# Optimization experiments

Hardware: AMD Instinct MI355X
Metric: run time of the kernel (lower is better)

The kernel has to match this reference:

```python
import math
import jax, jax.numpy as jnp
import numpy as np

EPS = 1e-4
FMAX = 18  # max filtersize for scale clamped to 2.5: ceil(3*2^2.5+0.5)=18 -> kernel 37x37
KSZ = 2 * FMAX + 1


def _conv2d(x, w, b):
    # 3x3 conv, padding 1, NCHW / OIHW (cross-correlation, matches torch)
    y = jax.lax.conv_general_dilated(x, w, (1, 1), [(1, 1), (1, 1)],
                                     dimension_numbers=('NCHW', 'OIHW', 'NCHW'))
    return y + b[None, :, None, None]


def _basis_filters(scale):
    # scale: [B] -> [B,3,K,K] (g, dgdx, dgdy), masked to the per-sample support
    std = 2.0 ** scale                              # [B]
    fs = jnp.ceil(3.0 * std + 0.5)                  # per-sample filtersize
    x = jnp.arange(-FMAX, FMAX + 1, dtype=jnp.float32)          # [K]
    m = (jnp.abs(x)[None, :] <= fs[:, None]).astype(jnp.float32)  # [B,K] support mask
    e = jnp.exp(-0.5 * (x[None, :] / std[:, None]) ** 2) * m      # masked 1D gaussian [B,K]
    g = e[:, :, None] * e[:, None, :]                              # [B,K,K]
    g = g / jnp.sum(g, axis=(1, 2), keepdims=True)
    c = (-x[None, :] / (std[:, None] ** 3 * 2.0 * math.pi)) * e    # [B,K]
    dgdx = c[:, :, None] * e[:, None, :]   # varies along first spatial dim (x[0])
    dgdx = dgdx / jnp.sum(jnp.abs(dgdx), axis=(1, 2), keepdims=True)
    dgdy = e[:, :, None] * c[:, None, :]   # varies along second spatial dim (x[1])
    dgdy = dgdy / jnp.sum(jnp.abs(dgdy), axis=(1, 2), keepdims=True)
    return jnp.stack([g, dgdx, dgdy], axis=1)  # [B,3,K,K]


def setup_inputs() -> dict:
    key = jax.random.key(0)
    ks = jax.random.split(key, 7)
    B, H, W = 8, 512, 512
    batch = jax.random.uniform(ks[0], (B, 3, H, W), dtype=jnp.float32)
    gcm = jnp.array([[0.06, 0.63, 0.27], [0.3, 0.04, -0.35], [0.34, -0.6, 0.17]],
                    dtype=jnp.float32)
    w1 = jax.random.normal(ks[1], (16, 3, 3, 3), dtype=jnp.float32) * 0.1
    b1 = jax.random.normal(ks[2], (16,), dtype=jnp.float32) * 0.01
    w2 = jax.random.normal(ks[3], (16, 16, 3, 3), dtype=jnp.float32) * 0.1
    b2 = jax.random.normal(ks[4], (16,), dtype=jnp.float32) * 0.01
    w3 = jax.random.normal(ks[5], (1, 16, 3, 3), dtype=jnp.float32) * 0.1
    b3 = jax.random.normal(ks[6], (1,), dtype=jnp.float32) * 0.01
    return {"batch": batch, "gcm": gcm, "w1": w1, "b1": b1,
            "w2": w2, "b2": b2, "w3": w3, "b3": b3}


def reference(batch, gcm, w1, b1, w2, b2, w3, b3):
    B, _, H, W = batch.shape
    # ---- RGB order prior (non-differentiable, no_grad in torch) ----
    oh = lambda i: jax.nn.one_hot(i, 3, axis=1, dtype=batch.dtype)
    mx = jnp.argmax(batch, axis=1)                 # first max
    mn = jnp.argmin(batch, axis=1)
    bf = batch[:, ::-1]
    mx2 = 2 - jnp.argmax(bf, axis=1)               # last max
    mn2 = 2 - jnp.argmin(bf, axis=1)
    RGB_order = jax.lax.stop_gradient(
        0.5 * (oh(mx) + oh(mx2)) - 0.5 * (oh(mn) + oh(mn2)))  # [B,3,H,W]

    # ---- per-sample adaptive scale from small CNN ----
    h = jax.nn.silu(_conv2d(batch, w1, b1))
    h = jax.nn.silu(_conv2d(h, w2, b2))
    s = _conv2d(h, w3, b3)
    scale = jnp.clip(jnp.mean(s, axis=(1, 2, 3)), -2.5, 2.5)   # [B]

    # ---- Gaussian color model ----
    xg = jnp.einsum('ij,bjhw->bihw', gcm, batch)  # [B,3,H,W] -> (E, El, Ell)

    # ---- per-sample Gaussian basis convolution, batched via grouped conv ----
    basis = _basis_filters(scale)                                  # [B,3,K,K]
    xin = xg.reshape(1, B * 3, H, W)
    wk = jnp.broadcast_to(basis[:, None], (B, 3, 3, KSZ, KSZ)).reshape(B * 9, 1, KSZ, KSZ)
    out = jax.lax.conv_general_dilated(xin, wk, (1, 1), [(FMAX, FMAX), (FMAX, FMAX)],
                                       feature_group_count=B * 3,
                                       dimension_numbers=('NCHW', 'OIHW', 'NCHW'))
    out = out.reshape(B, 3, 3, H, W)   # [B, chan(E/El/Ell), filt(g/dx/dy), H, W]
    E = out[:, 0, 0:1]
    Ex = out[:, 0, 1:2]
    Ey = out[:, 0, 2:3]
    El = out[:, 1, 0:1]
    Ell = out[:, 2, 0:1]

    Hf = jnp.arctan(El / (Ell + EPS))
    S = jnp.log((El ** 2 + Ell ** 2) / (E ** 2 + EPS) + EPS)
    Ww = jnp.arctan((Ex / (E + EPS)) ** 2 + (Ey / (E + EPS)) ** 2)
    return jnp.concatenate([Hf, S, RGB_order, Ww], axis=1)  # [B,6,H,W]
```

## Files before the change

kernel.cpp:

```cpp
#include <hip/hip_runtime.h>
#include <hip/hip_bf16.h>

constexpr int BN = 8, HH = 512, WW = 512;
constexpr int PIX = HH * WW;
constexpr float EPSF = 1e-4f;

__device__ __forceinline__ float b2f(__hip_bfloat16 x) { return __bfloat162float(x); }
__device__ __forceinline__ __hip_bfloat16 f2b(float x) { return __float2bfloat16(x); }
__device__ __forceinline__ unsigned short bfbits(float x) {
    union { __hip_bfloat16 b; unsigned short u; } cv; cv.b = f2b(x); return cv.u;
}
__device__ __forceinline__ unsigned int cvtpk(float lo, float hi) {
    unsigned int r;
    asm("v_cvt_pk_bf16_f32 %0, %1, %2" : "=v"(r) : "v"(lo), "v"(hi));
    return r;
}
__device__ __forceinline__ float silu(float a) {
    return a * __builtin_amdgcn_rcpf(1.f + __expf(-a));
}

typedef __attribute__((ext_vector_type(8))) short bf16x8;
typedef __attribute__((ext_vector_type(4))) float f32x4;

constexpr int OFF_TOT = 0;
constexpr int OFF_ROW0 = 128;
constexpr int OFF_ROW1 = 256;
constexpr int OFF_COL0 = 384;
constexpr int OFF_COL1 = 512;
constexpr int OFF_COR = 640;
constexpr int OFF_W1R = 1280;
constexpr int OFF_WR  = 2048;
constexpr int OFF_EH  = 4608;
constexpr int OFF_CH  = 5120;
constexpr size_t OFF_TPB = 65536;
constexpr size_t TP_BYTES = (size_t)4 * BN * PIX * 4;
constexpr size_t WS_NEEDED = OFF_TPB + TP_BYTES;

__global__ void prep_kernel(const float* __restrict__ w1, const float* __restrict__ w2,
                            float* __restrict__ wsf) {
    int t = threadIdx.x;
    for (int i = t; i < 640; i += 256) wsf[i] = 0.f;
    unsigned short* ab = (unsigned short*)(wsf + OFF_WR);
    for (int idx = t; idx < 5120; idx += 256) {
        int part = idx / 2560;
        int id = idx - part * 2560;
        int ks = id >> 9, rem = id & 511, lane = rem >> 3, j = id & 7;
        int oc = lane & 15, q = lane >> 4;
        int k = q * 8 + j;
        int tap = 2 * ks + (k >> 4), ic = k & 15;
        float val = (tap <= 8) ? w2[oc * 144 + ic * 9 + tap] : 0.f;
        float hv = b2f(f2b(val));
        ab[idx] = (part == 0) ? bfbits(val) : bfbits(val - hv);
    }
    unsigned short* a1 = (unsigned short*)(wsf + OFF_W1R);
    for (int idx = t; idx < 1024; idx += 256) {
        int part = idx >> 9;
        int id = idx & 511;
        int lane = id >> 3, j = id & 7;
        int oc = lane & 15, q = lane >> 4;
        int k = q * 8 + j;
        float val = (k < 27) ? w1[oc * 27 + k] : 0.f;
        float hv = b2f(f2b(val));
        a1[idx] = (part == 0) ? bfbits(val) : bfbits(val - hv);
    }
}

__global__ __launch_bounds__(256) void conv12_kernel(const float* __restrict__ batch,
                                                     const unsigned short* __restrict__ w1buf,
                                                     const float* __restrict__ b1,
                                                     const unsigned short* __restrict__ abuf,
                                                     const float* __restrict__ b2v,
                                                     float* __restrict__ wsf,
                                                     float* __restrict__ out) {
    __shared__ float st[3][12][68];
    __shared__ uint4 h1s[10 * 66 * 2];
    __shared__ float part[4][16];

    int tx = threadIdx.x;
    int lane = tx & 63, wave = tx >> 6;
    int n = lane & 15, q = lane >> 4;
    int w0 = blockIdx.x * 64, h0 = blockIdx.y * 8, b = blockIdx.z;

    union { uint4 u; bf16x8 v; } cv;
    const float* pb = batch + (size_t)(b * 3) * PIX;

    for (int i = tx; i < 2448; i += 256) {
        int ch = i / 816;
        int rem = i - ch * 816;
        int r = rem / 68, c = rem - r * 68;
        int gh = h0 - 2 + r, gw = w0 - 2 + c;
        float v = 0.f;
        if (gh >= 0 && gh < HH && gw >= 0 && gw < WW)
            v = pb[(size_t)ch * PIX + (size_t)gh * WW + gw];
        st[ch][r][c] = v;
    }

    bf16x8 w1h, w1l;
    const uint4* w14 = (const uint4*)w1buf;
    cv.u = w14[lane];      w1h = cv.v;
    cv.u = w14[64 + lane]; w1l = cv.v;
    int koff[8];
#pragma unroll
    for (int j = 0; j < 8; j++) {
        int k = q * 8 + j;
        int kk = (k < 27) ? k : 0;
        int ic = kk / 9, rem = kk - ic * 9, kh = rem / 3, kw = rem - kh * 3;
        koff[j] = ic * 816 + kh * 68 + kw;
    }
    float b1q[4];
#pragma unroll
    for (int r = 0; r < 4; r++) b1q[r] = b1[q * 4 + r];
    bool hiq = (q == 3);
    __syncthreads();

    const float* stf = &st[0][0][0];
    unsigned int* hw = (unsigned int*)h1s;
    for (int g = wave; g < 42; g += 4) {
        int i = g * 16 + n; if (i > 659) i = 659;
        int r = i / 66, c = i - r * 66;
        int base = r * 68 + c;
        float x[8];
#pragma unroll
        for (int j = 0; j < 8; j++) x[j] = stf[base + koff[j]];
#pragma unroll
        for (int j = 3; j < 8; j++) x[j] = hiq ? 0.f : x[j];
        union { unsigned int w[4]; bf16x8 v; } bb;
        bb.w[0] = cvtpk(x[0], x[1]);
        bb.w[1] = cvtpk(x[2], x[3]);
        bb.w[2] = cvtpk(x[4], x[5]);
        bb.w[3] = cvtpk(x[6], x[7]);
        f32x4 a = {0, 0, 0, 0};
        a = __builtin_amdgcn_mfma_f32_16x16x32_bf16(w1h, bb.v, a, 0, 0, 0);
        a = __builtin_amdgcn_mfma_f32_16x16x32_bf16(w1l, bb.v, a, 0, 0, 0);
        int gh = h0 - 1 + r, gw = w0 - 1 + c;
        bool ok = ((unsigned)gh < (unsigned)HH) && ((unsigned)gw < (unsigned)WW);
        unsigned int p0 = cvtpk(silu(a[0] + b1q[0]), silu(a[1] + b1q[1]));
        unsigned int p1 = cvtpk(silu(a[2] + b1q[2]), silu(a[3] + b1q[3]));
        p0 = ok ? p0 : 0u;
        p1 = ok ? p1 : 0u;
        int swz = (c >> 2) & 1;
        int slot = i * 2 + ((q >= 2) ? (swz ^ 1) : swz);
        *(uint2*)&hw[slot * 4 + (q & 1) * 2] = make_uint2(p0, p1);
    }

    for (int j = tx; j < 512; j += 256) {
        int rr = j >> 6, ccx = j & 63;
        float v0 = st[0][rr + 2][ccx + 2];
        float v1 = st[1][rr + 2][ccx + 2];
        float v2 = st[2][rr + 2][ccx + 2];
        int mx  = (v0 >= v1 && v0 >= v2) ? 0 : ((v1 >= v2) ? 1 : 2);
        int mx2 = (v2 >= v1 && v2 >= v0) ? 2 : ((v1 >= v0) ? 1 : 0);
        int mn  = (v0 <= v1 && v0 <= v2) ? 0 : ((v1 <= v2) ? 1 : 2);
        int mn2 = (v2 <= v1 && v2 <= v0) ? 2 : ((v1 <= v0) ? 1 : 0);
        size_t p = (size_t)(h0 + rr) * WW + (w0 + ccx);
#pragma unroll
        for (int c = 0; c < 3; c++) {
            float r = 0.5f * ((float)(c == mx) + (float)(c == mx2))
                    - 0.5f * ((float)(c == mn) + (float)(c == mn2));
            out[(size_t)(b * 6 + 2 + c) * PIX + p] = r;
        }
    }
    __syncthreads();

    bf16x8 ah[5], al[5];
    const uint4* ab4 = (const uint4*)abuf;
#pragma unroll
    for (int ks = 0; ks < 5; ks++) {
        cv.u = ab4[ks * 64 + lane];       ah[ks] = cv.v;
        cv.u = ab4[320 + ks * 64 + lane]; al[ks] = cv.v;
    }
    float b2q[4];
#pragma unroll
    for (int r = 0; r < 4; r++) b2q[r] = b2v[q * 4 + r];

    float tt[4] = {0, 0, 0, 0};
    float cs0[4] = {0, 0, 0, 0};
    float cs1[4] = {0, 0, 0, 0};
    for (int rloc = 0; rloc < 2; rloc++) {
        int row = wave * 2 + rloc;
        int grow = h0 + row;
        f32x4 acc[4] = {{0,0,0,0},{0,0,0,0},{0,0,0,0},{0,0,0,0}};
#pragma unroll
        for (int ks = 0; ks < 5; ks++) {
            int tap = 2 * ks + (q >> 1); if (tap > 8) tap = 8;
            int dh = tap / 3 - 1, dw = tap % 3 - 1;
            int half = q & 1;
            int lr = row + 1 + dh;
#pragma unroll
            for (int t = 0; t < 4; t++) {
                int c = 1 + dw + t * 16 + n;
                cv.u = h1s[(lr * 66 + c) * 2 + (half ^ ((c >> 2) & 1))];
                acc[t] = __builtin_amdgcn_mfma_f32_16x16x32_bf16(ah[ks], cv.v, acc[t], 0, 0, 0);
                acc[t] = __builtin_amdgcn_mfma_f32_16x16x32_bf16(al[ks], cv.v, acc[t], 0, 0, 0);
            }
        }
        float sv[4][4];
#pragma unroll
        for (int t = 0; t < 4; t++)
#pragma unroll
            for (int r = 0; r < 4; r++)
                sv[t][r] = silu(acc[t][r] + b2q[r]);
#pragma unroll
        for (int r = 0; r < 4; r++) tt[r] += sv[0][r] + sv[1][r] + sv[2][r] + sv[3][r];
        if (grow == 0 || grow == HH - 1) {
            int off = (grow == 0) ? OFF_ROW0 : OFF_ROW1;
#pragma unroll
            for (int r = 0; r < 4; r++) {
                float x = sv[0][r] + sv[1][r] + sv[2][r] + sv[3][r];
#pragma unroll
                for (int d = 1; d < 16; d <<= 1) x += __shfl_xor(x, d, 64);
                if (n == 0) atomicAdd(&wsf[off + b * 16 + q * 4 + r], x);
            }
        }
        if (blockIdx.x == 0 && n == 0)
#pragma unroll
            for (int r = 0; r < 4; r++) cs0[r] += sv[0][r];
        if (blockIdx.x == 7 && n == 15)
#pragma unroll
            for (int r = 0; r < 4; r++) cs1[r] += sv[3][r];
        if ((grow == 0 || grow == HH - 1)) {
            int hi = (grow == 0) ? 0 : 1;
            if (blockIdx.x == 0 && n == 0)
#pragma unroll
                for (int r = 0; r < 4; r++)
                    wsf[OFF_COR + ((b * 2 + hi) * 2 + 0) * 16 + q * 4 + r] = sv[0][r];
            if (blockIdx.x == 7 && n == 15)
#pragma unroll
                for (int r = 0; r < 4; r++)
                    wsf[OFF_COR + ((b * 2 + hi) * 2 + 1) * 16 + q * 4 + r] = sv[3][r];
        }
    }
    if (blockIdx.x == 0 && n == 0)
#pragma unroll
        for (int r = 0; r < 4; r++) atomicAdd(&wsf[OFF_COL0 + b * 16 + q * 4 + r], cs0[r]);
    if (blockIdx.x == 7 && n == 15)
#pragma unroll
        for (int r = 0; r < 4; r++) atomicAdd(&wsf[OFF_COL1 + b * 16 + q * 4 + r], cs1[r]);
#pragma unroll
    for (int r = 0; r < 4; r++) {
        float x = tt[r];
#pragma unroll
        for (int d = 1; d < 16; d <<= 1) x += __shfl_xor(x, d, 64);
        tt[r] = x;
    }
    if (n == 0)
#pragma unroll
        for (int r = 0; r < 4; r++) part[wave][q * 4 + r] = tt[r];
    __syncthreads();
    if (tx < 16)
        atomicAdd(&wsf[OFF_TOT + b * 16 + tx],
                  part[0][tx] + part[1][tx] + part[2][tx] + part[3][tx]);
}

__global__ void filter_kernel(const float* __restrict__ w3, const float* __restrict__ b3,
                              float* __restrict__ wsf) {
    int b = blockIdx.x, t = threadIdx.x;
    __shared__ float red[160];
    float val = 0.f;
    if (t < 144) {
        int ic = t / 9, tap = t % 9, kh = tap / 3, kw = tap % 3;
        float T = wsf[OFF_TOT + b * 16 + ic];
        int hi = -1, wi = -1;
        if (kh == 0) { T -= wsf[OFF_ROW1 + b * 16 + ic]; hi = 1; }
        else if (kh == 2) { T -= wsf[OFF_ROW0 + b * 16 + ic]; hi = 0; }
        if (kw == 0) { T -= wsf[OFF_COL1 + b * 16 + ic]; wi = 1; }
        else if (kw == 2) { T -= wsf[OFF_COL0 + b * 16 + ic]; wi = 0; }
        if (hi >= 0 && wi >= 0) T += wsf[OFF_COR + ((b * 2 + hi) * 2 + wi) * 16 + ic];
        val = w3[t] * T;
    }
    red[t] = val;
    __syncthreads();
    __shared__ float sh_mean;
    if (t == 0) {
        float S = 0.f;
        for (int i = 0; i < 144; i++) S += red[i];
        sh_mean = b3[0] + S * (1.f / (float)PIX);
    }
    __syncthreads();
    float scale = fminf(2.5f, fmaxf(-2.5f, sh_mean));
    float sd = exp2f(scale);
    float fs = ceilf(3.f * sd + 0.5f);
    float e = 0.f, c = 0.f;
    if (t < 37) {
        float x = (float)(t - 18);
        if (fabsf(x) <= fs) {
            float qq = x / sd;
            e = __expf(-0.5f * qq * qq);
            c = -x / (sd * sd * sd * 6.28318530717958647692f) * e;
        }
    }
    __shared__ float sa[40], sb[40];
    if (t < 37) { sa[t] = e; sb[t] = fabsf(c); }
    __syncthreads();
    __shared__ float Se, Sc;
    if (t == 0) {
        float a = 0.f, d = 0.f;
        for (int i = 0; i < 37; i++) { a += sa[i]; d += sb[i]; }
        Se = a; Sc = d;
    }
    __syncthreads();
    if (t < 37) {
        wsf[OFF_EH + b * 37 + t] = e / Se;
        wsf[OFF_CH + b * 37 + t] = c / Sc;
    }
}

__device__ __forceinline__ int skw(int c) { return c + (c >> 5); }
__global__ __launch_bounds__(256, 4) void horiz_kernel(const float* __restrict__ batch,
                                                       const float* __restrict__ gcm,
                                                       const float* __restrict__ ehat,
                                                       const float* __restrict__ chat,
                                                       float* __restrict__ t) {
    __shared__ float xr[2][3][566];
    int tx = threadIdx.x;
    int h0 = blockIdx.x * 2;
    int b  = blockIdx.y;
    const float* pb = batch + (size_t)(b * 3) * PIX;
    float g0 = gcm[0], g1 = gcm[1], g2 = gcm[2];
    float g3 = gcm[3], g4 = gcm[4], g5 = gcm[5];
    float g6 = gcm[6], g7 = gcm[7], g8 = gcm[8];
    for (int i = tx; i < 2 * 548; i += 256) {
        int r = i / 548, c = i - r * 548;
        int gw = c - 18;
        float v0 = 0.f, v1 = 0.f, v2 = 0.f;
        if (gw >= 0 && gw < WW) {
            size_t p = (size_t)(h0 + r) * WW + gw;
            v0 = pb[p]; v1 = pb[(size_t)PIX + p]; v2 = pb[2 * (size_t)PIX + p];
        }
        int cs = skw(c);
        xr[r][0][cs] = g0 * v0 + g1 * v1 + g2 * v2;
        xr[r][1][cs] = g3 * v0 + g4 * v1 + g5 * v2;
        xr[r][2][cs] = g6 * v0 + g7 * v1 + g8 * v2;
    }
    __syncthreads();
    int r = tx >> 7, colbase = (tx & 127) * 4;
    const float* eh = ehat + b * 37; const float* ch = chat + b * 37;
    float a0[4] = {}, a1[4] = {}, a2[4] = {}, a3[4] = {};
#pragma unroll 4
    for (int kk = 0; kk < 40; kk++) {
        int cs = skw(colbase + kk);
        float x0 = xr[r][0][cs], x1 = xr[r][1][cs], x2 = xr[r][2][cs];
#pragma unroll
        for (int i = 0; i < 4; i++) {
            int k = kk - i;
            if (k >= 0 && k < 37) {
                float ce = eh[k], cc = ch[k];
                a0[i] += ce * x0; a1[i] += ce * x1;
                a2[i] += ce * x2; a3[i] += cc * x0;
            }
        }
    }
    const size_t PL = (size_t)BN * PIX;
    size_t p = (size_t)b * PIX + (size_t)(h0 + r) * WW + colbase;
    *(float4*)&t[0 * PL + p] = make_float4(a0[0], a0[1], a0[2], a0[3]);
    *(float4*)&t[1 * PL + p] = make_float4(a1[0], a1[1], a1[2], a1[3]);
    *(float4*)&t[2 * PL + p] = make_float4(a2[0], a2[1], a2[2], a2[3]);
    *(float4*)&t[3 * PL + p] = make_float4(a3[0], a3[1], a3[2], a3[3]);
}

__global__ __launch_bounds__(256, 4) void vert_kernel(const float* __restrict__ t,
                                                      const float* __restrict__ ehat,
                                                      const float* __restrict__ chat,
                                                      float* __restrict__ out) {
    int tx = threadIdx.x;
    int j = blockIdx.x * 64 + (tx & 63);
    int r0 = (blockIdx.y * 4 + (tx >> 6)) * 4;
    int b = blockIdx.z;
    const float* eh = ehat + b * 37; const float* ch = chat + b * 37;
    const size_t PL = (size_t)BN * PIX;
    const float* t0 = t + (size_t)b * PIX;
    float E[4] = {}, Ex[4] = {}, Ey[4] = {}, El[4] = {}, Ell[4] = {};
#pragma unroll 4
    for (int kk = 0; kk < 40; kk++) {
        int gr = r0 - 18 + kk;
        if (gr >= 0 && gr < HH) {
            size_t idx = (size_t)gr * WW + j;
            float v0 = t0[idx], v1 = t0[PL + idx], v2 = t0[2 * PL + idx], v3 = t0[3 * PL + idx];
#pragma unroll
            for (int i = 0; i < 4; i++) {
                int k = kk - i;
                if (k >= 0 && k < 37) {
                    float ce = eh[k], cc = ch[k];
                    E[i] += ce * v0; Ex[i] += cc * v0; Ey[i] += ce * v3;
                    El[i] += ce * v1; Ell[i] += ce * v2;
                }
            }
        }
    }
#pragma unroll
    for (int i = 0; i < 4; i++) {
        int h = r0 + i;
        float Hf = atanf(El[i] / (Ell[i] + EPSF));
        float S = logf((El[i] * El[i] + Ell[i] * Ell[i]) / (E[i] * E[i] + EPSF) + EPSF);
        float rx = Ex[i] / (E[i] + EPSF), ry = Ey[i] / (E[i] + EPSF);
        float Wv = atanf(rx * rx + ry * ry);
        size_t base = (size_t)(b * 6) * PIX + (size_t)h * WW + j;
        out[base] = Hf;
        out[base + PIX] = S;
        out[base + 5 * (size_t)PIX] = Wv;
    }
}

extern "C" void kernel_launch(void* const* d_in, const int* in_sizes, int n_in,
                              void* d_out, int out_size, void* d_ws, size_t ws_size,
                              hipStream_t stream) {
    const float* batch = (const float*)d_in[0];
    const float* gcm   = (const float*)d_in[1];
    const float* w1    = (const float*)d_in[2];
    const float* b1    = (const float*)d_in[3];
    const float* w2    = (const float*)d_in[4];
    const float* b2    = (const float*)d_in[5];
    const float* w3    = (const float*)d_in[6];
    const float* b3    = (const float*)d_in[7];
    float* out = (float*)d_out;

    if (ws_size < WS_NEEDED) return;

    float* wsf = (float*)d_ws;
    float* tpl = (float*)((char*)d_ws + OFF_TPB);
    float* ehat = wsf + OFF_EH;
    float* chat = wsf + OFF_CH;

    prep_kernel<<<dim3(1), dim3(256), 0, stream>>>(w1, w2, wsf);
    conv12_kernel<<<dim3(8, 64, 8), dim3(256), 0, stream>>>(
        batch, (const unsigned short*)(wsf + OFF_W1R), b1,
        (const unsigned short*)(wsf + OFF_WR), b2, wsf, out);
    filter_kernel<<<dim3(8), dim3(160), 0, stream>>>(w3, b3, wsf);
    horiz_kernel<<<dim3(256, 8), dim3(256), 0, stream>>>(batch, gcm, ehat, chat, tpl);
    vert_kernel<<<dim3(8, 32, 8), dim3(256), 0, stream>>>(tpl, ehat, chat, out);
}
```

Measured before the change: 251.5 us.

## Peel separable conv loops, rotate coefficients in registers, add interior fast paths

The horizontal and vertical Gaussian passes now stage the per-sample filter taps in shared memory. Each pass peels its 40-step tap loop into prologue, steady-state and epilogue parts, passing the taps to the four output rows or columns through rotating registers, which removes the per-iteration bounds and index checks. The vertical pass adds an interior-block path with no row-bounds checks. The conv12 kernel loads input rows one per wave, with unchecked loads for non-edge blocks, and its first-layer loop is reorganised by rows so border masking only runs in edge blocks. In exchange there is more code and register pressure, plus one extra block barrier in the vertical kernel.

```diff
diff --git a/kernel.cpp b/kernel.cpp
--- a/kernel.cpp
+++ b/kernel.cpp
@@ -80,19 +80,29 @@
     int lane = tx & 63, wave = tx >> 6;
     int n = lane & 15, q = lane >> 4;
     int w0 = blockIdx.x * 64, h0 = blockIdx.y * 8, b = blockIdx.z;
+    bool edgeB = (blockIdx.x == 0) || (blockIdx.x == 7) || (blockIdx.y == 0) || (blockIdx.y == 63);
 
     union { uint4 u; bf16x8 v; } cv;
     const float* pb = batch + (size_t)(b * 3) * PIX;
 
-    for (int i = tx; i < 2448; i += 256) {
-        int ch = i / 816;
-        int rem = i - ch * 816;
-        int r = rem / 68, c = rem - r * 68;
-        int gh = h0 - 2 + r, gw = w0 - 2 + c;
-        float v = 0.f;
-        if (gh >= 0 && gh < HH && gw >= 0 && gw < WW)
-            v = pb[(size_t)ch * PIX + (size_t)gh * WW + gw];
-        st[ch][r][c] = v;
+    for (int rr = wave; rr < 36; rr += 4) {
+        int ch = rr / 12, r = rr - ch * 12;
+        int gh = h0 - 2 + r;
+        const float* rp = pb + (size_t)ch * PIX + (size_t)gh * WW + (w0 - 2);
+        if (!edgeB) {
+            st[ch][r][lane] = rp[lane];
+            if (lane < 4) st[ch][r][64 + lane] = rp[64 + lane];
+        } else {
+            bool rok = (gh >= 0) && (gh < HH);
+            int gw = w0 - 2 + lane;
+            float v = (rok && gw >= 0 && gw < WW) ? rp[lane] : 0.f;
+            st[ch][r][lane] = v;
+            if (lane < 4) {
+                int gw2 = gw + 64;
+                float v2 = (rok && gw2 >= 0 && gw2 < WW) ? rp[64 + lane] : 0.f;
+                st[ch][r][64 + lane] = v2;
+            }
+        }
     }
 
     bf16x8 w1h, w1l;
@@ -111,14 +121,16 @@
 #pragma unroll
     for (int r = 0; r < 4; r++) b1q[r] = b1[q * 4 + r];
     bool hiq = (q == 3);
+    int swzl = (n >> 2) & 1;
     __syncthreads();
 
     const float* stf = &st[0][0][0];
     unsigned int* hw = (unsigned int*)h1s;
-    for (int g = wave; g < 42; g += 4) {
-        int i = g * 16 + n; if (i > 659) i = 659;
-        int r = i / 66, c = i - r * 66;
-        int base = r * 68 + c;
+    for (int g = wave; g < 50; g += 4) {
+        int row = g / 5, sub = g - row * 5;
+        int c = sub * 16 + n;
+        int cc_ = (c < 66) ? c : 65;
+        int base = row * 68 + cc_;
         float x[8];
 #pragma unroll
         for (int j = 0; j < 8; j++) x[j] = stf[base + koff[j]];
@@ -132,15 +144,18 @@
         f32x4 a = {0, 0, 0, 0};
         a = __builtin_amdgcn_mfma_f32_16x16x32_bf16(w1h, bb.v, a, 0, 0, 0);
         a = __builtin_amdgcn_mfma_f32_16x16x32_bf16(w1l, bb.v, a, 0, 0, 0);
-        int gh = h0 - 1 + r, gw = w0 - 1 + c;
-        bool ok = ((unsigned)gh < (unsigned)HH) && ((unsigned)gw < (unsigned)WW);
         unsigned int p0 = cvtpk(silu(a[0] + b1q[0]), silu(a[1] + b1q[1]));
         unsigned int p1 = cvtpk(silu(a[2] + b1q[2]), silu(a[3] + b1q[3]));
-        p0 = ok ? p0 : 0u;
-        p1 = ok ? p1 : 0u;
-        int swz = (c >> 2) & 1;
-        int slot = i * 2 + ((q >= 2) ? (swz ^ 1) : swz);
-        *(uint2*)&hw[slot * 4 + (q & 1) * 2] = make_uint2(p0, p1);
+        if (edgeB) {
+            int gh = h0 - 1 + row, gw = w0 - 1 + cc_;
+            bool ok = (gh >= 0) && (gh < HH) && (gw >= 0) && (gw < WW);
+            p0 = ok ? p0 : 0u;
+            p1 = ok ? p1 : 0u;
+        }
+        if (c < 66) {
+            int slot = (row * 66 + c) * 2 + ((q >= 2) ? (swzl ^ 1) : swzl);
+            *(uint2*)&hw[slot * 4 + (q & 1) * 2] = make_uint2(p0, p1);
+        }
     }
 
     for (int j = tx; j < 512; j += 256) {
@@ -312,9 +327,11 @@
                                                        const float* __restrict__ chat,
                                                        float* __restrict__ t) {
     __shared__ float xr[2][3][566];
+    __shared__ float cE[40], cC[40];
     int tx = threadIdx.x;
     int h0 = blockIdx.x * 2;
     int b  = blockIdx.y;
+    if (tx < 37) { cE[tx] = ehat[b * 37 + tx]; cC[tx] = chat[b * 37 + tx]; }
     const float* pb = batch + (size_t)(b * 3) * PIX;
     float g0 = gcm[0], g1 = gcm[1], g2 = gcm[2];
     float g3 = gcm[3], g4 = gcm[4], g5 = gcm[5];
@@ -334,21 +351,56 @@
     }
     __syncthreads();
     int r = tx >> 7, colbase = (tx & 127) * 4;
-    const float* eh = ehat + b * 37; const float* ch = chat + b * 37;
     float a0[4] = {}, a1[4] = {}, a2[4] = {}, a3[4] = {};
-#pragma unroll 4
-    for (int kk = 0; kk < 40; kk++) {
+    float e1, e2, e3, d1, d2, d3;
+    {
+        float ce[3], cc2[3];
+#pragma unroll
+        for (int k = 0; k < 3; k++) { ce[k] = cE[k]; cc2[k] = cC[k]; }
+#pragma unroll
+        for (int kk = 0; kk < 3; kk++) {
+            int cs = skw(colbase + kk);
+            float x0 = xr[r][0][cs], x1 = xr[r][1][cs], x2 = xr[r][2][cs];
+#pragma unroll
+            for (int i = 0; i < 3; i++) {
+                if (i <= kk) {
+                    float ce_ = ce[kk - i], cc_ = cc2[kk - i];
+                    a0[i] += ce_ * x0; a1[i] += ce_ * x1;
+                    a2[i] += ce_ * x2; a3[i] += cc_ * x0;
+                }
+            }
+        }
+        e1 = ce[2]; e2 = ce[1]; e3 = ce[0];
+        d1 = cc2[2]; d2 = cc2[1]; d3 = cc2[0];
+    }
+#pragma unroll 2
+    for (int kk = 3; kk < 37; kk++) {
+        float e0 = cE[kk], d0 = cC[kk];
         int cs = skw(colbase + kk);
         float x0 = xr[r][0][cs], x1 = xr[r][1][cs], x2 = xr[r][2][cs];
-#pragma unroll
-        for (int i = 0; i < 4; i++) {
-            int k = kk - i;
-            if (k >= 0 && k < 37) {
-                float ce = eh[k], cc = ch[k];
-                a0[i] += ce * x0; a1[i] += ce * x1;
-                a2[i] += ce * x2; a3[i] += cc * x0;
-            }
-        }
+        a0[0] += e0 * x0; a1[0] += e0 * x1; a2[0] += e0 * x2; a3[0] += d0 * x0;
+        a0[1] += e1 * x0; a1[1] += e1 * x1; a2[1] += e1 * x2; a3[1] += d1 * x0;
+        a0[2] += e2 * x0; a1[2] += e2 * x1; a2[2] += e2 * x2; a3[2] += d2 * x0;
+        a0[3] += e3 * x0; a1[3] += e3 * x1; a2[3] += e3 * x2; a3[3] += d3 * x0;
+        e3 = e2; e2 = e1; e1 = e0; d3 = d2; d2 = d1; d1 = d0;
+    }
+    {
+        int cs = skw(colbase + 37);
+        float x0 = xr[r][0][cs], x1 = xr[r][1][cs], x2 = xr[r][2][cs];
+        a0[1] += e1 * x0; a1[1] += e1 * x1; a2[1] += e1 * x2; a3[1] += d1 * x0;
+        a0[2] += e2 * x0; a1[2] += e2 * x1; a2[2] += e2 * x2; a3[2] += d2 * x0;
+        a0[3] += e3 * x0; a1[3] += e3 * x1; a2[3] += e3 * x2; a3[3] += d3 * x0;
+    }
+    {
+        int cs = skw(colbase + 38);
+        float x0 = xr[r][0][cs], x1 = xr[r][1][cs], x2 = xr[r][2][cs];
+        a0[2] += e1 * x0; a1[2] += e1 * x1; a2[2] += e1 * x2; a3[2] += d1 * x0;
+        a0[3] += e2 * x0; a1[3] += e2 * x1; a2[3] += e2 * x2; a3[3] += d2 * x0;
+    }
+    {
+        int cs = skw(colbase + 39);
+        float x0 = xr[r][0][cs], x1 = xr[r][1][cs], x2 = xr[r][2][cs];
+        a0[3] += e1 * x0; a1[3] += e1 * x1; a2[3] += e1 * x2; a3[3] += d1 * x0;
     }
     const size_t PL = (size_t)BN * PIX;
     size_t p = (size_t)b * PIX + (size_t)(h0 + r) * WW + colbase;
@@ -358,34 +410,82 @@
     *(float4*)&t[3 * PL + p] = make_float4(a3[0], a3[1], a3[2], a3[3]);
 }
 
+#define VACC(ee, dd, ii) { E[ii] += (ee) * v0; Ex[ii] += (dd) * v0; Ey[ii] += (ee) * v3; \
+                           El[ii] += (ee) * v1; Ell[ii] += (ee) * v2; }
 __global__ __launch_bounds__(256, 4) void vert_kernel(const float* __restrict__ t,
                                                       const float* __restrict__ ehat,
                                                       const float* __restrict__ chat,
                                                       float* __restrict__ out) {
+    __shared__ float cE[40], cC[40];
     int tx = threadIdx.x;
+    int b = blockIdx.z;
+    if (tx < 37) { cE[tx] = ehat[b * 37 + tx]; cC[tx] = chat[b * 37 + tx]; }
     int j = blockIdx.x * 64 + (tx & 63);
     int r0 = (blockIdx.y * 4 + (tx >> 6)) * 4;
-    int b = blockIdx.z;
-    const float* eh = ehat + b * 37; const float* ch = chat + b * 37;
     const size_t PL = (size_t)BN * PIX;
     const float* t0 = t + (size_t)b * PIX;
+    __syncthreads();
     float E[4] = {}, Ex[4] = {}, Ey[4] = {}, El[4] = {}, Ell[4] = {};
-#pragma unroll 4
-    for (int kk = 0; kk < 40; kk++) {
+    bool safe = (r0 >= 18) && (r0 <= HH - 22);
+    float e1, e2, e3, d1, d2, d3;
+    {
+        float ce[3], cc2[3];
+#pragma unroll
+        for (int k = 0; k < 3; k++) { ce[k] = cE[k]; cc2[k] = cC[k]; }
+#pragma unroll
+        for (int kk = 0; kk < 3; kk++) {
+            int gr = r0 - 18 + kk;
+            float v0 = 0.f, v1 = 0.f, v2 = 0.f, v3 = 0.f;
+            if ((unsigned)gr < (unsigned)HH) {
+                size_t idx = (size_t)gr * WW + j;
+                v0 = t0[idx]; v1 = t0[PL + idx]; v2 = t0[2 * PL + idx]; v3 = t0[3 * PL + idx];
+            }
+#pragma unroll
+            for (int i = 0; i < 3; i++) {
+                if (i <= kk) {
+                    float ee = ce[kk - i], dd = cc2[kk - i];
+                    VACC(ee, dd, i)
+                }
+            }
+        }
+        e1 = ce[2]; e2 = ce[1]; e3 = ce[0];
+        d1 = cc2[2]; d2 = cc2[1]; d3 = cc2[0];
+    }
+    const float* pv = t0 + (size_t)(r0 - 15) * WW + j;
+    if (safe) {
+#pragma unroll 2
+        for (int kk = 3; kk < 37; kk++) {
+            float e0 = cE[kk], d0 = cC[kk];
+            float v0 = pv[0], v1 = pv[PL], v2 = pv[2 * PL], v3 = pv[3 * PL];
+            VACC(e0, d0, 0) VACC(e1, d1, 1) VACC(e2, d2, 2) VACC(e3, d3, 3)
+            e3 = e2; e2 = e1; e1 = e0; d3 = d2; d2 = d1; d1 = d0;
+            pv += WW;
+        }
+    } else {
+        int gr = r0 - 15;
+#pragma unroll 2
+        for (int kk = 3; kk < 37; kk++) {
+            float e0 = cE[kk], d0 = cC[kk];
+            float v0 = 0.f, v1 = 0.f, v2 = 0.f, v3 = 0.f;
+            if ((unsigned)gr < (unsigned)HH) {
+                v0 = pv[0]; v1 = pv[PL]; v2 = pv[2 * PL]; v3 = pv[3 * PL];
+            }
+            VACC(e0, d0, 0) VACC(e1, d1, 1) VACC(e2, d2, 2) VACC(e3, d3, 3)
+            e3 = e2; e2 = e1; e1 = e0; d3 = d2; d2 = d1; d1 = d0;
+            pv += WW; gr++;
+        }
+    }
+#pragma unroll
+    for (int kk = 37; kk < 40; kk++) {
         int gr = r0 - 18 + kk;
-        if (gr >= 0 && gr < HH) {
+        float v0 = 0.f, v1 = 0.f, v2 = 0.f, v3 = 0.f;
+        if (gr < HH) {
             size_t idx = (size_t)gr * WW + j;
-            float v0 = t0[idx], v1 = t0[PL + idx], v2 = t0[2 * PL + idx], v3 = t0[3 * PL + idx];
-#pragma unroll
-            for (int i = 0; i < 4; i++) {
-                int k = kk - i;
-                if (k >= 0 && k < 37) {
-                    float ce = eh[k], cc = ch[k];
-                    E[i] += ce * v0; Ex[i] += cc * v0; Ey[i] += ce * v3;
-                    El[i] += ce * v1; Ell[i] += ce * v2;
-                }
-            }
-        }
+            v0 = t0[idx]; v1 = t0[PL + idx]; v2 = t0[2 * PL + idx]; v3 = t0[3 * PL + idx];
+        }
+        if (kk == 37) { VACC(e1, d1, 1) VACC(e2, d2, 2) VACC(e3, d3, 3) }
+        if (kk == 38) { VACC(e1, d1, 2) VACC(e2, d2, 3) }
+        if (kk == 39) { VACC(e1, d1, 3) }
     }
 #pragma unroll
     for (int i = 0; i < 4; i++) {
@@ -400,6 +500,7 @@
         out[base + 5 * (size_t)PIX] = Wv;
     }
 }
+#undef VACC
 
 extern "C" void kernel_launch(void* const* d_in, const int* in_sizes, int n_in,
                               void* d_out, int out_size, void* d_ws, size_t ws_size,
```

New measurement: 259.0 us. +3.0%, slower.
